# Optimization experiments

Measured on AMD Instinct MI355X. Metric: run time of the kernel, lower is better.

## Reference

```python
import jax, jax.numpy as jnp
import numpy as np

B, C, N, CIN, COUT, ORDER = 16, 32, 207, 64, 64, 2
SCALE = COUT / (ORDER * CIN)          # = 0.5
BN_EVAL = 1.0 / np.sqrt(1.0 + 1e-5)   # eval-mode BatchNorm2d at init (mean=0, var=1)


def setup_inputs() -> dict:
    key = jax.random.key(0)
    ks = jax.random.split(key, 9)
    s = 0.05  # xavier-ish small init scale
    return {
        "x":          jax.random.normal(ks[0], (B, C, N, CIN), dtype=jnp.float32),
        "res_weight": jax.random.normal(ks[1], (C, N, CIN, COUT, ORDER), dtype=jnp.float32) * s,
        "res_bias":   jax.random.normal(ks[2], (1, C, N, 1, 1), dtype=jnp.float32) * s,
        "mlp_w":      jax.random.normal(ks[3], (COUT, CIN), dtype=jnp.float32) * s,
        "mlp_b":      jax.random.normal(ks[4], (COUT,), dtype=jnp.float32) * s,
        "gate_w":     jax.random.normal(ks[5], (COUT, CIN), dtype=jnp.float32) * s,
        "gate_b":     jax.random.normal(ks[6], (COUT,), dtype=jnp.float32) * s,
        "order_w":    jax.random.normal(ks[7], (ORDER,), dtype=jnp.float32) * s,
        "order_b":    jax.random.normal(ks[8], (1,), dtype=jnp.float32) * s,
    }


def reference(x, res_weight, res_bias, mlp_w, mlp_b, gate_w, gate_b, order_w, order_b):
    # shared linear branch (dropout = identity in eval)
    x_share = jnp.einsum('bcni,oi->bcno', x, mlp_w) + mlp_b            # [B,C,N,COUT]
    # polynomial features: h[..., 0]=x, h[..., 1]=BN(x*x) (eval BN ~ identity scale)
    x1 = (x * x) * BN_EVAL
    h = jnp.stack([x, x1], axis=-1)                                    # [B,C,N,CIN,ORDER]
    # per-(channel,node) grouped linear
    x_uniq = jnp.einsum('bcnid,cniod->bcnod', h, res_weight) + res_bias  # [B,C,N,COUT,ORDER]
    # order_mlp: Linear(order -> 1), squeeze
    x_uniq = jnp.einsum('bcnod,d->bcno', x_uniq, order_w) + order_b    # [B,C,N,COUT]
    x_uniq = x_uniq * (SCALE / 4.0)
    # sigmoid gate combine + residual
    gate = jax.nn.sigmoid(jnp.einsum('bcni,oi->bcno', x, gate_w) + gate_b)
    return gate * x_uniq + (1.0 - gate) * x_share + x
```

## Files before the change

### kernel.cpp

```cpp
#include <hip/hip_runtime.h>

#define Bdim 16
#define Cdim 32
#define Ndim 207
#define X_B (Cdim * Ndim * 64)
#define X_C (Ndim * 64)
#define W_C (Ndim * 64 * 64 * 2)
#define W_N (64 * 64 * 2)
#define BN_EVAL 0.9999950000374997f

using s8v = __attribute__((ext_vector_type(8))) short;
using f4v = __attribute__((ext_vector_type(4))) float;

union UV { uint4 u; s8v s; };

__device__ __forceinline__ unsigned pk(float lo, float hi) {
    union { float f; unsigned u; } a, b;
    a.f = lo; b.f = hi;
    return __builtin_amdgcn_perm(b.u, a.u, 0x07060302u);
}

__global__ __launch_bounds__(256, 4)
void fused_ml_mfma(const float* __restrict__ x,
                   const float* __restrict__ rw,
                   const float* __restrict__ rb,
                   const float* __restrict__ mw,
                   const float* __restrict__ mb,
                   const float* __restrict__ gw,
                   const float* __restrict__ gb,
                   const float* __restrict__ ow,
                   const float* __restrict__ obp,
                   float* __restrict__ out)
{
    __shared__ unsigned short A1[16 * 136];
    __shared__ unsigned short A2[16 * 72];
    __shared__ unsigned short MG[128 * 72];

    const int cn = blockIdx.x, c = cn / Ndim, n = cn % Ndim;
    const int t = threadIdx.x;
    const float ow0 = ow[0], ow1 = ow[1];
    const float bnow1 = ow1 * BN_EVAL;

    {
        const int b = t >> 4, i0 = (t & 15) * 4;
        const float* xrow = x + (size_t)b * X_B + (size_t)c * X_C + n * 64;
        const float4 xv = *(const float4*)(xrow + i0);
        uint4 v;
        v.x = pk(xv.x * ow0, xv.x * xv.x * bnow1);
        v.y = pk(xv.y * ow0, xv.y * xv.y * bnow1);
        v.z = pk(xv.z * ow0, xv.z * xv.z * bnow1);
        v.w = pk(xv.w * ow0, xv.w * xv.w * bnow1);
        *(uint4*)&A1[b * 136 + i0 * 2] = v;
        uint2 p;
        p.x = pk(xv.x, xv.y);
        p.y = pk(xv.z, xv.w);
        *(uint2*)&A2[b * 72 + i0] = p;
    }
    {
        const int r = t >> 1, h = t & 1;
        const float* src = (r < 64 ? mw + r * 64 : gw + (r - 64) * 64) + h * 32;
        unsigned short* dst = &MG[r * 72 + h * 32];
#pragma unroll
        for (int u = 0; u < 4; ++u) {
            const float4 a4 = ((const float4*)src)[2 * u];
            const float4 b4 = ((const float4*)src)[2 * u + 1];
            uint4 v;
            v.x = pk(a4.x, a4.y); v.y = pk(a4.z, a4.w);
            v.z = pk(b4.x, b4.y); v.w = pk(b4.z, b4.w);
            *(uint4*)&dst[u * 8] = v;
        }
    }
    __syncthreads();

    const int l = t & 63, w = t >> 6, q = l >> 4, nn = l & 15;
    const int o = w * 16 + nn;
    const float* wtile = rw + (size_t)c * W_C + (size_t)n * W_N + o * 2;

    f4v accU = {0.f, 0.f, 0.f, 0.f};
    f4v accM = {0.f, 0.f, 0.f, 0.f};
    f4v accG = {0.f, 0.f, 0.f, 0.f};

#pragma unroll
    for (int s = 0; s < 4; ++s) {
        const float* gp = wtile + (size_t)(16 * s + 4 * q) * 128;
        const float2 w0 = *(const float2*)(gp);
        const float2 w1 = *(const float2*)(gp + 128);
        const float2 w2 = *(const float2*)(gp + 256);
        const float2 w3 = *(const float2*)(gp + 384);
        UV bu;
        bu.u.x = pk(w0.x, w0.y); bu.u.y = pk(w1.x, w1.y);
        bu.u.z = pk(w2.x, w2.y); bu.u.w = pk(w3.x, w3.y);
        UV au; au.u = *(const uint4*)&A1[nn * 136 + 32 * s + 8 * q];
        accU = __builtin_amdgcn_mfma_f32_16x16x32_bf16(au.s, bu.s, accU, 0, 0, 0);
    }
#pragma unroll
    for (int s = 0; s < 2; ++s) {
        UV a2u; a2u.u = *(const uint4*)&A2[nn * 72 + 32 * s + 8 * q];
        UV bm;  bm.u  = *(const uint4*)&MG[o * 72 + 32 * s + 8 * q];
        UV bg2; bg2.u = *(const uint4*)&MG[(64 + o) * 72 + 32 * s + 8 * q];
        accM = __builtin_amdgcn_mfma_f32_16x16x32_bf16(a2u.s, bm.s,  accM, 0, 0, 0);
        accG = __builtin_amdgcn_mfma_f32_16x16x32_bf16(a2u.s, bg2.s, accG, 0, 0, 0);
    }

    const float rbias = rb[c * Ndim + n];
    const float uconst = rbias * (ow0 + ow1) + obp[0];
    const float mbias = mb[o], gbias = gb[o];
    const float* xcol = x + (size_t)c * X_C + n * 64 + o;
    float* ocol = out + (size_t)c * X_C + n * 64 + o;
#pragma unroll
    for (int r = 0; r < 4; ++r) {
        const int b = q * 4 + r;
        const float uniq = (accU[r] + uconst) * 0.125f;
        const float xs = accM[r] + mbias;
        const float g = 1.f / (1.f + __expf(-(accG[r] + gbias)));
        const float xres = xcol[(size_t)b * X_B];
        ocol[(size_t)b * X_B] = g * uniq + (1.f - g) * xs + xres;
    }
}

extern "C" void kernel_launch(void* const* d_in, const int* in_sizes, int n_in,
                              void* d_out, int out_size, void* d_ws, size_t ws_size,
                              hipStream_t stream)
{
    const float* x   = (const float*)d_in[0];
    const float* rw  = (const float*)d_in[1];
    const float* rb  = (const float*)d_in[2];
    const float* mw  = (const float*)d_in[3];
    const float* mb  = (const float*)d_in[4];
    const float* gw  = (const float*)d_in[5];
    const float* gb  = (const float*)d_in[6];
    const float* ow  = (const float*)d_in[7];
    const float* ob  = (const float*)d_in[8];
    float* out = (float*)d_out;

    fused_ml_mfma<<<dim3(Cdim * Ndim), dim3(256), 0, stream>>>(
        x, rw, rb, mw, mb, gw, gb, ow, ob, out);
}
```

Measured before the change: 333.5 us.

## Process four (c,n) tiles per block with register double-buffered weight prefetch

Each block now handles four consecutive (c,n) pairs instead of one. The next tile's res_weight slice and x row are prefetched into registers while the current tile's MFMAs run, and the A operands sit in double-buffered LDS. The mlp/gate weights are loaded once per block straight into MFMA B-operand registers rather than staged through LDS, which removes the per-block staging cost and the 18KB LDS array. The price is higher register pressure (launch bounds drop to 3 waves per SIMD) and 4x fewer blocks, which may hurt latency hiding on a bandwidth-bound kernel.

```diff
diff --git a/kernel.cpp b/kernel.cpp
--- a/kernel.cpp
+++ b/kernel.cpp
@@ -1,12 +1,9 @@
 #include <hip/hip_runtime.h>
 
-#define Bdim 16
-#define Cdim 32
-#define Ndim 207
-#define X_B (Cdim * Ndim * 64)
-#define X_C (Ndim * 64)
-#define W_C (Ndim * 64 * 64 * 2)
-#define W_N (64 * 64 * 2)
+#define X_B (32 * 207 * 64)
+#define NCN (32 * 207)
+#define NT 4
+#define NBLK (NCN / NT)
 #define BN_EVAL 0.9999950000374997f
 
 using s8v = __attribute__((ext_vector_type(8))) short;
@@ -20,7 +17,88 @@
     return __builtin_amdgcn_perm(b.u, a.u, 0x07060302u);
 }
 
-__global__ __launch_bounds__(256, 4)
+__device__ __forceinline__ void lds_barrier() {
+    asm volatile("s_waitcnt lgkmcnt(0)" ::: "memory");
+    __builtin_amdgcn_s_barrier();
+}
+
+#define TILE(K, WCUR, WNXT, CUR, NXT, LAST)                                      \
+    {                                                                            \
+        const int cn = cn0 + (K);                                                \
+                        \
+        float4 xnv;                                                              \
+        if (!(LAST)) xnv = *(const float4*)(xstage_base + ((K) + 1) * 64);       \
+                \
+            \
+        const float* xcol = x + (size_t)cn * 64 + o;                             \
+        float xres0 = xcol[(size_t)(q * 4 + 0) * X_B];                           \
+        float xres1 = xcol[(size_t)(q * 4 + 1) * X_B];                           \
+        float xres2 = xcol[(size_t)(q * 4 + 2) * X_B];                           \
+        float xres3 = xcol[(size_t)(q * 4 + 3) * X_B];                           \
+        __builtin_amdgcn_sched_barrier(0);  \
+        if (!(LAST)) {                                                           \
+            const float* wt = rw + (size_t)(cn + 1) * 8192 + o * 2 + 4 * q * 128;\
+            _Pragma("unroll")                                                    \
+            for (int u = 0; u < 16; ++u)                                         \
+                WNXT[u] = *(const float2*)(wt + (size_t)((u >> 2) * 16 + (u & 3)) * 128); \
+        }                                                                        \
+        f4v accU = {0.f, 0.f, 0.f, 0.f};                                         \
+        f4v accM = {0.f, 0.f, 0.f, 0.f};                                         \
+        f4v accG = {0.f, 0.f, 0.f, 0.f};                                         \
+         \
+        _Pragma("unroll")                                                        \
+        for (int s = 0; s < 4; ++s) {                                            \
+            UV bu;                                                               \
+            bu.u.x = pk(WCUR[s * 4 + 0].x, WCUR[s * 4 + 0].y);                   \
+            bu.u.y = pk(WCUR[s * 4 + 1].x, WCUR[s * 4 + 1].y);                   \
+            bu.u.z = pk(WCUR[s * 4 + 2].x, WCUR[s * 4 + 2].y);                   \
+            bu.u.w = pk(WCUR[s * 4 + 3].x, WCUR[s * 4 + 3].y);                   \
+            UV au; au.u = *(const uint4*)&A1[CUR][nn * 136 + 32 * s + 8 * q];    \
+            accU = __builtin_amdgcn_mfma_f32_16x16x32_bf16(au.s, bu.s, accU, 0, 0, 0); \
+        }                                                                        \
+            \
+        {                                                                        \
+            UV a2u0; a2u0.u = *(const uint4*)&A2[CUR][nn * 72 + 8 * q];          \
+            accM = __builtin_amdgcn_mfma_f32_16x16x32_bf16(a2u0.s, bmf0.s, accM, 0, 0, 0); \
+            accG = __builtin_amdgcn_mfma_f32_16x16x32_bf16(a2u0.s, bgf0.s, accG, 0, 0, 0); \
+            UV a2u1; a2u1.u = *(const uint4*)&A2[CUR][nn * 72 + 32 + 8 * q];     \
+            accM = __builtin_amdgcn_mfma_f32_16x16x32_bf16(a2u1.s, bmf1.s, accM, 0, 0, 0); \
+            accG = __builtin_amdgcn_mfma_f32_16x16x32_bf16(a2u1.s, bgf1.s, accG, 0, 0, 0); \
+        }                                                                        \
+                                           \
+        const float uconst = rb[cn] * (ow0 + ow1) + ob0;                         \
+        float* ocol = out + (size_t)cn * 64 + o;                                 \
+        {                                                                        \
+            const float u0 = (accU[0] + uconst) * 0.125f;                        \
+            const float u1 = (accU[1] + uconst) * 0.125f;                        \
+            const float u2 = (accU[2] + uconst) * 0.125f;                        \
+            const float u3 = (accU[3] + uconst) * 0.125f;                        \
+            const float s0 = accM[0] + mbias, s1 = accM[1] + mbias;              \
+            const float s2 = accM[2] + mbias, s3 = accM[3] + mbias;              \
+            const float g0 = 1.f / (1.f + __expf(-(accG[0] + gbias)));           \
+            const float g1 = 1.f / (1.f + __expf(-(accG[1] + gbias)));           \
+            const float g2 = 1.f / (1.f + __expf(-(accG[2] + gbias)));           \
+            const float g3 = 1.f / (1.f + __expf(-(accG[3] + gbias)));           \
+            ocol[(size_t)(q * 4 + 0) * X_B] = g0 * u0 + (1.f - g0) * s0 + xres0; \
+            ocol[(size_t)(q * 4 + 1) * X_B] = g1 * u1 + (1.f - g1) * s1 + xres1; \
+            ocol[(size_t)(q * 4 + 2) * X_B] = g2 * u2 + (1.f - g2) * s2 + xres2; \
+            ocol[(size_t)(q * 4 + 3) * X_B] = g3 * u3 + (1.f - g3) * s3 + xres3; \
+        }                                                                        \
+               \
+        if (!(LAST)) {                                                           \
+            uint4 v;                                                             \
+            v.x = pk(xnv.x * ow0, xnv.x * xnv.x * bnow1);                        \
+            v.y = pk(xnv.y * ow0, xnv.y * xnv.y * bnow1);                        \
+            v.z = pk(xnv.z * ow0, xnv.z * xnv.z * bnow1);                        \
+            v.w = pk(xnv.w * ow0, xnv.w * xnv.w * bnow1);                        \
+            *(uint4*)&A1[NXT][sb * 136 + si0 * 2] = v;                           \
+            uint2 p; p.x = pk(xnv.x, xnv.y); p.y = pk(xnv.z, xnv.w);             \
+            *(uint2*)&A2[NXT][sb * 72 + si0] = p;                                \
+            lds_barrier();                                                       \
+        }                                                                        \
+    }
+
+__global__ __launch_bounds__(256, 3)
 void fused_ml_mfma(const float* __restrict__ x,
                    const float* __restrict__ rw,
                    const float* __restrict__ rb,
@@ -32,90 +110,66 @@
                    const float* __restrict__ obp,
                    float* __restrict__ out)
 {
-    __shared__ unsigned short A1[16 * 136];
-    __shared__ unsigned short A2[16 * 72];
-    __shared__ unsigned short MG[128 * 72];
+    __shared__ unsigned short A1[2][16 * 136];
+    __shared__ unsigned short A2[2][16 * 72];
 
-    const int cn = blockIdx.x, c = cn / Ndim, n = cn % Ndim;
+    const int cn0 = blockIdx.x * NT;
     const int t = threadIdx.x;
     const float ow0 = ow[0], ow1 = ow[1];
     const float bnow1 = ow1 * BN_EVAL;
 
+    const int l = t & 63, w = t >> 6, q = l >> 4, nn = l & 15;
+    const int o = w * 16 + nn;
+    const int sb = t >> 4, si0 = (t & 15) * 4;
+
+    const float* xstage_base = x + (size_t)sb * X_B + (size_t)cn0 * 64 + si0;
+
+    const float4 xv = *(const float4*)xstage_base;
+    const float* mrow = mw + o * 64 + 8 * q;
+    const float* grow = gw + o * 64 + 8 * q;
+    const float4 m00 = *(const float4*)(mrow);
+    const float4 m01 = *(const float4*)(mrow + 4);
+    const float4 m10 = *(const float4*)(mrow + 32);
+    const float4 m11 = *(const float4*)(mrow + 36);
+    const float4 g00 = *(const float4*)(grow);
+    const float4 g01 = *(const float4*)(grow + 4);
+    const float4 g10 = *(const float4*)(grow + 32);
+    const float4 g11 = *(const float4*)(grow + 36);
+    __builtin_amdgcn_sched_barrier(0);
+    float2 wb0[16], wb1[16];
     {
-        const int b = t >> 4, i0 = (t & 15) * 4;
-        const float* xrow = x + (size_t)b * X_B + (size_t)c * X_C + n * 64;
-        const float4 xv = *(const float4*)(xrow + i0);
+        const float* wt = rw + (size_t)cn0 * 8192 + o * 2 + 4 * q * 128;
+#pragma unroll
+        for (int u = 0; u < 16; ++u)
+            wb0[u] = *(const float2*)(wt + (size_t)((u >> 2) * 16 + (u & 3)) * 128);
+    }
+    UV bmf0, bmf1, bgf0, bgf1;
+    bmf0.u.x = pk(m00.x, m00.y); bmf0.u.y = pk(m00.z, m00.w);
+    bmf0.u.z = pk(m01.x, m01.y); bmf0.u.w = pk(m01.z, m01.w);
+    bmf1.u.x = pk(m10.x, m10.y); bmf1.u.y = pk(m10.z, m10.w);
+    bmf1.u.z = pk(m11.x, m11.y); bmf1.u.w = pk(m11.z, m11.w);
+    bgf0.u.x = pk(g00.x, g00.y); bgf0.u.y = pk(g00.z, g00.w);
+    bgf0.u.z = pk(g01.x, g01.y); bgf0.u.w = pk(g01.z, g01.w);
+    bgf1.u.x = pk(g10.x, g10.y); bgf1.u.y = pk(g10.z, g10.w);
+    bgf1.u.z = pk(g11.x, g11.y); bgf1.u.w = pk(g11.z, g11.w);
+    const float mbias = mb[o], gbias = gb[o], ob0 = obp[0];
+
+    {
         uint4 v;
         v.x = pk(xv.x * ow0, xv.x * xv.x * bnow1);
         v.y = pk(xv.y * ow0, xv.y * xv.y * bnow1);
         v.z = pk(xv.z * ow0, xv.z * xv.z * bnow1);
         v.w = pk(xv.w * ow0, xv.w * xv.w * bnow1);
-        *(uint4*)&A1[b * 136 + i0 * 2] = v;
-        uint2 p;
-        p.x = pk(xv.x, xv.y);
-        p.y = pk(xv.z, xv.w);
-        *(uint2*)&A2[b * 72 + i0] = p;
+        *(uint4*)&A1[0][sb * 136 + si0 * 2] = v;
+        uint2 p; p.x = pk(xv.x, xv.y); p.y = pk(xv.z, xv.w);
+        *(uint2*)&A2[0][sb * 72 + si0] = p;
     }
-    {
-        const int r = t >> 1, h = t & 1;
-        const float* src = (r < 64 ? mw + r * 64 : gw + (r - 64) * 64) + h * 32;
-        unsigned short* dst = &MG[r * 72 + h * 32];
-#pragma unroll
-        for (int u = 0; u < 4; ++u) {
-            const float4 a4 = ((const float4*)src)[2 * u];
-            const float4 b4 = ((const float4*)src)[2 * u + 1];
-            uint4 v;
-            v.x = pk(a4.x, a4.y); v.y = pk(a4.z, a4.w);
-            v.z = pk(b4.x, b4.y); v.w = pk(b4.z, b4.w);
-            *(uint4*)&dst[u * 8] = v;
-        }
-    }
-    __syncthreads();
+    lds_barrier();
 
-    const int l = t & 63, w = t >> 6, q = l >> 4, nn = l & 15;
-    const int o = w * 16 + nn;
-    const float* wtile = rw + (size_t)c * W_C + (size_t)n * W_N + o * 2;
-
-    f4v accU = {0.f, 0.f, 0.f, 0.f};
-    f4v accM = {0.f, 0.f, 0.f, 0.f};
-    f4v accG = {0.f, 0.f, 0.f, 0.f};
-
-#pragma unroll
-    for (int s = 0; s < 4; ++s) {
-        const float* gp = wtile + (size_t)(16 * s + 4 * q) * 128;
-        const float2 w0 = *(const float2*)(gp);
-        const float2 w1 = *(const float2*)(gp + 128);
-        const float2 w2 = *(const float2*)(gp + 256);
-        const float2 w3 = *(const float2*)(gp + 384);
-        UV bu;
-        bu.u.x = pk(w0.x, w0.y); bu.u.y = pk(w1.x, w1.y);
-        bu.u.z = pk(w2.x, w2.y); bu.u.w = pk(w3.x, w3.y);
-        UV au; au.u = *(const uint4*)&A1[nn * 136 + 32 * s + 8 * q];
-        accU = __builtin_amdgcn_mfma_f32_16x16x32_bf16(au.s, bu.s, accU, 0, 0, 0);
-    }
-#pragma unroll
-    for (int s = 0; s < 2; ++s) {
-        UV a2u; a2u.u = *(const uint4*)&A2[nn * 72 + 32 * s + 8 * q];
-        UV bm;  bm.u  = *(const uint4*)&MG[o * 72 + 32 * s + 8 * q];
-        UV bg2; bg2.u = *(const uint4*)&MG[(64 + o) * 72 + 32 * s + 8 * q];
-        accM = __builtin_amdgcn_mfma_f32_16x16x32_bf16(a2u.s, bm.s,  accM, 0, 0, 0);
-        accG = __builtin_amdgcn_mfma_f32_16x16x32_bf16(a2u.s, bg2.s, accG, 0, 0, 0);
-    }
-
-    const float rbias = rb[c * Ndim + n];
-    const float uconst = rbias * (ow0 + ow1) + obp[0];
-    const float mbias = mb[o], gbias = gb[o];
-    const float* xcol = x + (size_t)c * X_C + n * 64 + o;
-    float* ocol = out + (size_t)c * X_C + n * 64 + o;
-#pragma unroll
-    for (int r = 0; r < 4; ++r) {
-        const int b = q * 4 + r;
-        const float uniq = (accU[r] + uconst) * 0.125f;
-        const float xs = accM[r] + mbias;
-        const float g = 1.f / (1.f + __expf(-(accG[r] + gbias)));
-        const float xres = xcol[(size_t)b * X_B];
-        ocol[(size_t)b * X_B] = g * uniq + (1.f - g) * xs + xres;
-    }
+    TILE(0, wb0, wb1, 0, 1, false)
+    TILE(1, wb1, wb0, 1, 0, false)
+    TILE(2, wb0, wb1, 0, 1, false)
+    TILE(3, wb1, wb0, 1, 0, true)
 }
 
 extern "C" void kernel_launch(void* const* d_in, const int* in_sizes, int n_in,
@@ -133,6 +187,6 @@
     const float* ob  = (const float*)d_in[8];
     float* out = (float*)d_out;
 
-    fused_ml_mfma<<<dim3(Cdim * Ndim), dim3(256), 0, stream>>>(
+    fused_ml_mfma<<<dim3(NBLK), dim3(256), 0, stream>>>(
         x, rw, rb, mw, mb, gw, gb, ow, ob, out);
 }
```

Measured after the change: 338.2 us. No clear change (+1.4%).
